# Performance work log

Measured on AMD Instinct MI355X. Metric: run time of the kernel, lower is better.

Reference implementation:

```python
import jax, jax.numpy as jnp
import numpy as np

DIM = 1024
HEADS = 16
DIM_HEAD = 64
INNER = HEADS * DIM_HEAD  # 1024
EPS = 1e-5


def layernorm(x, w, b):
    mu = jnp.mean(x, axis=-1, keepdims=True)
    var = jnp.mean(jnp.square(x - mu), axis=-1, keepdims=True)
    return (x - mu) * jax.lax.rsqrt(var + EPS) * w + b


def setup_inputs() -> dict:
    key = jax.random.key(0)
    ks = jax.random.split(key, 9)
    b, n1, n2 = 4, 4096, 256
    x = jax.random.normal(ks[0], (b, n1, DIM), dtype=jnp.float32)
    latents = jax.random.normal(ks[1], (b, n2, DIM), dtype=jnp.float32)
    shift = jax.random.normal(ks[2], (b, HEADS), dtype=jnp.float32)
    scale = jax.random.normal(ks[3], (b, HEADS), dtype=jnp.float32)
    s = 1.0 / np.sqrt(DIM)
    Wq = jax.random.normal(ks[4], (DIM, INNER), dtype=jnp.float32) * s
    Wkv = jax.random.normal(ks[5], (DIM, 2 * INNER), dtype=jnp.float32) * s
    Wout = jax.random.normal(ks[6], (INNER, DIM), dtype=jnp.float32) * (1.0 / np.sqrt(INNER))
    ln1_w = jnp.ones((DIM,), jnp.float32)
    ln1_b = jnp.zeros((DIM,), jnp.float32)
    ln2_w = jnp.ones((DIM,), jnp.float32)
    ln2_b = jnp.zeros((DIM,), jnp.float32)
    return {"x": x, "latents": latents, "shift": shift, "scale": scale,
            "ln1_w": ln1_w, "ln1_b": ln1_b, "ln2_w": ln2_w, "ln2_b": ln2_b,
            "Wq": Wq, "Wkv": Wkv, "Wout": Wout}


def reference(x, latents, shift, scale, ln1_w, ln1_b, ln2_w, ln2_b, Wq, Wkv, Wout):
    b = x.shape[0]
    xn = layernorm(x, ln1_w, ln1_b)            # (b, n1, D)
    ln = layernorm(latents, ln2_w, ln2_b)      # (b, n2, D)
    q = ln @ Wq                                 # (b, n2, inner)
    kv = xn @ Wkv                               # (b, n1, 2*inner)
    k, v = jnp.split(kv, 2, axis=-1)
    q = q.reshape(b, -1, HEADS, DIM_HEAD)
    k = k.reshape(b, -1, HEADS, DIM_HEAD)
    v = v.reshape(b, -1, HEADS, DIM_HEAD)
    # AdaLN-style per-head modulation on q
    q = q * (1.0 + scale[:, None, :, None]) + shift[:, None, :, None]
    # fp32 attention scores (already fp32 here)
    attn_scale = DIM_HEAD ** -0.5
    qk = jnp.einsum('bihd,bjhd->bhij', q.astype(jnp.float32), k.astype(jnp.float32)) * attn_scale
    attn = jax.nn.softmax(qk, axis=-1).astype(v.dtype)  # (b, h, n2, n1)
    out = jnp.einsum('bhij,bjhd->bihd', attn, v)         # (b, n2, h, dh)
    out = out.reshape(b, -1, INNER)
    return out @ Wout
```

## Files before the change

### kernel.cpp

```cpp
#include <hip/hip_runtime.h>

typedef __bf16 bf16;
typedef bf16 bf16x8 __attribute__((ext_vector_type(8)));
typedef bf16 bf16x4 __attribute__((ext_vector_type(4)));
typedef float f32x4 __attribute__((ext_vector_type(4)));

#define B_ 4
#define N1 4096
#define N2 256
#define DIM 1024
#define HEADS 16
#define DH 64
#define INNER 1024
#define ASPLIT 4
#define KEYS_PER_SPLIT (N1 / ASPLIT)
#define SPLIT_ELEMS (4 * 16 * 256 * 64)

typedef __attribute__((address_space(1))) const void gvoid_t;
typedef __attribute__((address_space(3))) void lvoid_t;
__device__ __forceinline__ void async16(const void* g, void* l) {
  __builtin_amdgcn_global_load_lds((gvoid_t*)g, (lvoid_t*)l, 16, 0, 0);
}

__global__ __launch_bounds__(256) void ln_all(
    const float* __restrict__ x, const float* __restrict__ latents,
    const float* __restrict__ ln1w, const float* __restrict__ ln1b,
    const float* __restrict__ ln2w, const float* __restrict__ ln2b,
    bf16* __restrict__ xn, bf16* __restrict__ lnl) {
  int wv = threadIdx.x >> 6, lane = threadIdx.x & 63;
  int grow = blockIdx.x * 4 + wv;
  const float *src, *w, *bb;
  bf16* dst;
  int row;
  if (grow < 16384) { src = x; w = ln1w; bb = ln1b; dst = xn; row = grow; }
  else { src = latents; w = ln2w; bb = ln2b; dst = lnl; row = grow - 16384; }
  const float4* p = (const float4*)(src + (size_t)row * DIM);
  float4 v[4];
  for (int j = 0; j < 4; j++) v[j] = p[j * 64 + lane];
  float s = 0.f, sq = 0.f;
  for (int j = 0; j < 4; j++) {
    s += v[j].x + v[j].y + v[j].z + v[j].w;
    sq += v[j].x * v[j].x + v[j].y * v[j].y + v[j].z * v[j].z + v[j].w * v[j].w;
  }
  for (int off = 32; off; off >>= 1) {
    s += __shfl_xor(s, off, 64);
    sq += __shfl_xor(sq, off, 64);
  }
  float mu = s * (1.0f / DIM);
  float var = sq * (1.0f / DIM) - mu * mu;
  float r = rsqrtf(var + 1e-5f);
  for (int j = 0; j < 4; j++) {
    float4 wv4 = ((const float4*)w)[j * 64 + lane];
    float4 bv4 = ((const float4*)bb)[j * 64 + lane];
    bf16x4 o;
    o[0] = (bf16)((v[j].x - mu) * r * wv4.x + bv4.x);
    o[1] = (bf16)((v[j].y - mu) * r * wv4.y + bv4.y);
    o[2] = (bf16)((v[j].z - mu) * r * wv4.z + bv4.z);
    o[3] = (bf16)((v[j].w - mu) * r * wv4.w + bv4.w);
    *(bf16x4*)(dst + (size_t)row * DIM + (j * 64 + lane) * 4) = o;
  }
}

__global__ __launch_bounds__(256) void transpose_w_all(
    const float* __restrict__ Wq, const float* __restrict__ Wkv,
    const float* __restrict__ Wout, bf16* __restrict__ WqT,
    bf16* __restrict__ WkvT, bf16* __restrict__ WoutT) {
  __shared__ float tile[32][33];
  int t = blockIdx.x;
  const float* src;
  bf16* dst;
  int N;
  if (t < 1024) { src = Wq; dst = WqT; N = 1024; }
  else if (t < 3072) { t -= 1024; src = Wkv; dst = WkvT; N = 2048; }
  else { t -= 3072; src = Wout; dst = WoutT; N = 1024; }
  int ntiles = N >> 5;
  int n0 = (t % ntiles) * 32, k0 = (t / ntiles) * 32;
  int x = threadIdx.x, y = threadIdx.y;
  for (int j = 0; j < 4; j++)
    tile[y + 8 * j][x] = src[(size_t)(k0 + y + 8 * j) * N + n0 + x];
  __syncthreads();
  for (int j = 0; j < 4; j++)
    dst[(size_t)(n0 + y + 8 * j) * 1024 + k0 + x] = (bf16)tile[x][y + 8 * j];
}

__global__ __launch_bounds__(256) void gemm_kv(
    const bf16* __restrict__ A, const bf16* __restrict__ Bt,
    bf16* __restrict__ Cout, bf16* __restrict__ Cout2, int K) {
  __shared__ __align__(16) bf16 smem[128 * 64 * 2];
  bf16* As = smem;
  bf16* Bs = smem + 128 * 64;
  int tid = threadIdx.x;
  int lane = tid & 63, wv = tid >> 6;
  int wr = wv >> 1, wc = wv & 1;
  int quad = lane >> 4, lr = lane & 15;
  int bid = blockIdx.y * 16 + blockIdx.x;
  int c = bid & 7, g = bid >> 3;
  int mi = g & 7, nb = (g >> 3) & 15, chunk = g >> 7;
  int m0 = (chunk * 64 + mi * 8 + c) * 128;
  int n0 = nb * 128;
  f32x4 acc[4][4] = {};
  for (int kt = 0; kt < K; kt += 64) {
    __syncthreads();
    for (int j = 0; j < 4; j++) {
      int idx0 = j * 256 + wv * 64;
      int row = (idx0 >> 3) + (lane >> 3);
      int cb = (lane & 7) ^ (row & 7);
      async16(&A[(size_t)(m0 + row) * K + kt + cb * 8], &As[idx0 * 8]);
      async16(&Bt[(size_t)(n0 + row) * K + kt + cb * 8], &Bs[idx0 * 8]);
    }
    __syncthreads();
    for (int kk = 0; kk < 2; kk++) {
      bf16x8 af[4], bfr[4];
      for (int im = 0; im < 4; im++) {
        int row = wr * 64 + im * 16 + lr;
        af[im] = *(const bf16x8*)&As[row * 64 + ((quad + 4 * kk) ^ (row & 7)) * 8];
      }
      for (int in = 0; in < 4; in++) {
        int row = wc * 64 + in * 16 + lr;
        bfr[in] = *(const bf16x8*)&Bs[row * 64 + ((quad + 4 * kk) ^ (row & 7)) * 8];
      }
      for (int im = 0; im < 4; im++)
        for (int in = 0; in < 4; in++)
          acc[im][in] = __builtin_amdgcn_mfma_f32_16x16x32_bf16(
              af[im], bfr[in], acc[im][in], 0, 0, 0);
    }
  }

  if (n0 >= 1024) {
    bf16* Ct = smem;
    for (int pass = 0; pass < 2; pass++) {
      __syncthreads();
      for (int inL = 0; inL < 2; inL++) {
        int in = pass * 2 + inL;
        int cc = wc * 32 + inL * 16 + lr;
        for (int im = 0; im < 4; im++) {
          int rb = wr * 64 + im * 16 + quad * 4;
          bf16x4 pk;
          for (int r = 0; r < 4; r++) pk[r] = (bf16)acc[im][in][r];
          *(bf16x4*)&Ct[cc * 136 + rb] = pk;
        }
      }
      __syncthreads();
      for (int k2 = 0; k2 < 4; k2++) {
        int ci = k2 * 256 + tid;
        int cc = ci >> 4, ch = ci & 15;
        uint4 val = *(const uint4*)&Ct[cc * 136 + ch * 8];
        int gco = (cc >> 5) * 64 + pass * 32 + (cc & 31);
        int col = n0 - 1024 + gco;
        int bb2 = m0 >> 12;
        int key = (m0 & 4095) + ch * 8;
        *(uint4*)&Cout2[((size_t)(bb2 * 1024 + col)) * 4096 + key] = val;
      }
    }
    return;
  }

  for (int im = 0; im < 4; im++)
    for (int in = 0; in < 4; in++) {
      int col = n0 + wc * 64 + in * 16 + lr;
      for (int r = 0; r < 4; r++) {
        int row = m0 + wr * 64 + im * 16 + quad * 4 + r;
        Cout[(size_t)row * 1024 + col] = (bf16)acc[im][in][r];
      }
    }
}

template <int MODE>
__global__ __launch_bounds__(256) void gemm64(
    const bf16* __restrict__ A, const bf16* __restrict__ Bt,
    void* __restrict__ Cout, int K, int N,
    const float* __restrict__ shiftp, const float* __restrict__ scalep) {
  __shared__ __align__(16) bf16 As[64 * 64];
  __shared__ __align__(16) bf16 Bs[64 * 64];
  int tid = threadIdx.x;
  int lane = tid & 63, wv = tid >> 6;
  int wr = wv >> 1, wc = wv & 1;
  int quad = lane >> 4, lr = lane & 15;
  int m0 = blockIdx.y * 64, n0 = blockIdx.x * 64;
  f32x4 acc[2][2] = {};
  for (int kt = 0; kt < K; kt += 64) {
    __syncthreads();
    for (int j = 0; j < 2; j++) {
      int idx0 = j * 256 + wv * 64;
      int row = (idx0 >> 3) + (lane >> 3);
      int cb = (lane & 7) ^ (row & 7);
      async16(&A[(size_t)(m0 + row) * K + kt + cb * 8], &As[idx0 * 8]);
      async16(&Bt[(size_t)(n0 + row) * K + kt + cb * 8], &Bs[idx0 * 8]);
    }
    __syncthreads();
    for (int kk = 0; kk < 2; kk++) {
      bf16x8 af[2], bfr[2];
      for (int im = 0; im < 2; im++) {
        int row = wr * 32 + im * 16 + lr;
        af[im] = *(const bf16x8*)&As[row * 64 + ((quad + 4 * kk) ^ (row & 7)) * 8];
      }
      for (int in = 0; in < 2; in++) {
        int row = wc * 32 + in * 16 + lr;
        bfr[in] = *(const bf16x8*)&Bs[row * 64 + ((quad + 4 * kk) ^ (row & 7)) * 8];
      }
      for (int im = 0; im < 2; im++)
        for (int in = 0; in < 2; in++)
          acc[im][in] = __builtin_amdgcn_mfma_f32_16x16x32_bf16(
              af[im], bfr[in], acc[im][in], 0, 0, 0);
    }
  }
  for (int im = 0; im < 2; im++)
    for (int in = 0; in < 2; in++) {
      int col = n0 + wc * 32 + in * 16 + lr;
      for (int r = 0; r < 4; r++) {
        int row = m0 + wr * 32 + im * 16 + quad * 4 + r;
        float v = acc[im][in][r];
        if (MODE == 1) {
          int bb = row >> 8, hh = col >> 6;
          float sc = scalep[bb * 16 + hh], sh = shiftp[bb * 16 + hh];
          ((bf16*)Cout)[(size_t)row * N + col] =
              (bf16)((v * (1.0f + sc) + sh) * 0.18033688011112042f);
        } else {
          ((float*)Cout)[(size_t)row * N + col] = v;
        }
      }
    }
}

__global__ __launch_bounds__(256) void attn_kernel(const bf16* __restrict__ q,
                                                   const bf16* __restrict__ kb,
                                                   const bf16* __restrict__ vt,
                                                   float* __restrict__ opA,
                                                   float* __restrict__ opB,
                                                   float* __restrict__ ml) {
  int b = blockIdx.z, h = blockIdx.y;
  int qt = blockIdx.x >> 2, sp = blockIdx.x & 3;
  int tid = threadIdx.x, lane = tid & 63, wv = tid >> 6;
  int quad = lane >> 4, lr = lane & 15;
  __shared__ __align__(16) bf16 Ks[64 * 64];
  __shared__ __align__(16) bf16 Vs[64 * 64];
  __shared__ __align__(16) bf16 QP[64 * 64];
  __shared__ float abuf[4][16];
  int q0 = qt * 64;

  const bf16* qg = q + (size_t)(b * N2 + q0) * INNER + h * DH;
  for (int j = 0; j < 2; j++) {
    int r0 = j * 32 + wv * 8;
    int r = r0 + (lane >> 3);
    async16(&qg[(size_t)r * INNER + ((lane & 7) ^ (r & 7)) * 8], &QP[r0 * 64]);
  }
  __syncthreads();
  bf16x8 aQ[2];
  {
    int row = wv * 16 + lr;
    for (int kk = 0; kk < 2; kk++)
      aQ[kk] = *(const bf16x8*)&QP[row * 64 + ((quad + 4 * kk) ^ (row & 7)) * 8];
  }
  float m_s = -1e30f, l_s = 0.0f;
  f32x4 oacc[4] = {};

  const bf16* kg = kb + (size_t)(b * N1) * 1024 + h * DH;
  const bf16* vg = vt + (size_t)((b * HEADS + h) * DH) * N1;
  bf16* Ps = QP + wv * 1024;

  for (int t = 0; t < KEYS_PER_SPLIT / 64; t++) {
    int key0 = sp * KEYS_PER_SPLIT + t * 64;
    __syncthreads();
    for (int j = 0; j < 2; j++) {
      int r0 = j * 32 + wv * 8;
      int r = r0 + (lane >> 3);
      int cs = ((lane & 7) ^ (r & 7)) * 8;
      async16(&kg[(size_t)(key0 + r) * 1024 + cs], &Ks[r0 * 64]);
      async16(&vg[(size_t)r * N1 + key0 + cs], &Vs[r0 * 64]);
    }
    __syncthreads();

    f32x4 s[4] = {};
    for (int kk = 0; kk < 2; kk++)
      for (int nt = 0; nt < 4; nt++) {
        int row = nt * 16 + lr;
        bf16x8 ak =
            *(const bf16x8*)&Ks[row * 64 + ((quad + 4 * kk) ^ (row & 7)) * 8];
        s[nt] = __builtin_amdgcn_mfma_f32_16x16x32_bf16(ak, aQ[kk], s[nt], 0, 0, 0);
      }

    float mx = s[0][0];
    for (int nt = 0; nt < 4; nt++)
      for (int r = 0; r < 4; r++) mx = fmaxf(mx, s[nt][r]);
    mx = fmaxf(mx, __shfl_xor(mx, 16, 64));
    mx = fmaxf(mx, __shfl_xor(mx, 32, 64));
    float mn = fmaxf(m_s, mx);
    float al = exp2f(m_s - mn);
    float p[4][4], sum = 0.0f;
    for (int nt = 0; nt < 4; nt++)
      for (int r = 0; r < 4; r++) {
        p[nt][r] = exp2f(s[nt][r] - mn);
        sum += p[nt][r];
      }
    sum += __shfl_xor(sum, 16, 64);
    sum += __shfl_xor(sum, 32, 64);
    l_s = l_s * al + sum;
    m_s = mn;
    if (quad == 0) abuf[wv][lr] = al;

    for (int nt = 0; nt < 4; nt++) {
      bf16x4 pk;
      for (int r = 0; r < 4; r++) pk[r] = (bf16)p[nt][r];
      *(bf16x4*)&Ps[lr * 64 + ((2 * nt + (quad >> 1)) ^ (lr & 7)) * 8 +
                    (quad & 1) * 4] = pk;
    }

    f32x4 a4 = *(const f32x4*)&abuf[wv][quad * 4];
    for (int in = 0; in < 4; in++)
      for (int r = 0; r < 4; r++) oacc[in][r] *= a4[r];

    bf16x8 aP[2];
    for (int kk = 0; kk < 2; kk++)
      aP[kk] = *(const bf16x8*)&Ps[lr * 64 + ((4 * kk + quad) ^ (lr & 7)) * 8];

    for (int kk = 0; kk < 2; kk++)
      for (int in = 0; in < 4; in++) {
        int row = in * 16 + lr;
        bf16x8 bv =
            *(const bf16x8*)&Vs[row * 64 + ((quad + 4 * kk) ^ (row & 7)) * 8];
        oacc[in] = __builtin_amdgcn_mfma_f32_16x16x32_bf16(aP[kk], bv, oacc[in], 0, 0, 0);
      }
  }

  float* ob = (sp < 2 ? opA : opB) + (size_t)(sp & 1) * SPLIT_ELEMS;
  size_t rbase = (size_t)(b * HEADS + h) * N2;
  for (int r = 0; r < 4; r++) {
    int qq = q0 + wv * 16 + quad * 4 + r;
    for (int in = 0; in < 4; in++)
      ob[(rbase + qq) * 64 + in * 16 + lr] = oacc[in][r];
  }
  if (quad == 0) {
    int qq = q0 + wv * 16 + lr;
    float* mlp = ml + ((size_t)sp * (4 * HEADS * N2) + rbase + qq) * 2;
    mlp[0] = m_s;
    mlp[1] = l_s;
  }
}

__global__ __launch_bounds__(256) void combine_kernel(const float* __restrict__ opA,
                                                      const float* __restrict__ opB,
                                                      const float* __restrict__ ml,
                                                      bf16* __restrict__ out) {
  int gid = blockIdx.x * 256 + threadIdx.x;
  int d = gid & 63;
  int rq = gid >> 6;
  int qq = rq & 255, bh = rq >> 8;
  int h = bh & 15, b = bh >> 4;
  float m[ASPLIT], l[ASPLIT];
  for (int s = 0; s < ASPLIT; s++) {
    const float* p = ml + ((size_t)s * (4 * HEADS * N2) + rq) * 2;
    m[s] = p[0];
    l[s] = p[1];
  }
  float M = fmaxf(fmaxf(m[0], m[1]), fmaxf(m[2], m[3]));
  float L = 0.0f, o = 0.0f;
  for (int s = 0; s < ASPLIT; s++) {
    float w = exp2f(m[s] - M);
    L += w * l[s];
    const float* op = (s < 2 ? opA : opB) + (size_t)(s & 1) * SPLIT_ELEMS;
    o += w * op[(size_t)rq * 64 + d];
  }
  out[((size_t)(b * N2 + qq)) * INNER + h * DH + d] = (bf16)(o / L);
}

extern "C" void kernel_launch(void* const* d_in, const int* in_sizes, int n_in,
                              void* d_out, int out_size, void* d_ws,
                              size_t ws_size, hipStream_t stream) {
  const float* x       = (const float*)d_in[0];
  const float* latents = (const float*)d_in[1];
  const float* shift   = (const float*)d_in[2];
  const float* scale   = (const float*)d_in[3];
  const float* ln1w    = (const float*)d_in[4];
  const float* ln1b    = (const float*)d_in[5];
  const float* ln2w    = (const float*)d_in[6];
  const float* ln2b    = (const float*)d_in[7];
  const float* Wq      = (const float*)d_in[8];
  const float* Wkv     = (const float*)d_in[9];
  const float* Wout    = (const float*)d_in[10];

  char* ws = (char*)d_ws;
  bf16*  xn    = (bf16*)(ws);
  float* opA   = (float*)(ws);
  bf16*  lnl   = (bf16*)(ws + 33554432);
  float* ml    = (float*)(ws + 33554432);
  bf16*  qb    = (bf16*)(ws + 35651584);
  bf16*  kb    = (bf16*)(ws + 37748736);
  float* opB   = (float*)(ws + 71303168);
  bf16*  vtb   = (bf16*)(ws + 104857600);
  bf16*  aob   = (bf16*)(ws + 138412032);
  bf16*  WqT   = (bf16*)(ws + 140509184);
  bf16*  WkvT  = (bf16*)(ws + 142606336);
  bf16*  WoutT = (bf16*)(ws + 146800640);

  transpose_w_all<<<4096, dim3(32, 8), 0, stream>>>(Wq, Wkv, Wout, WqT, WkvT,
                                                    WoutT);
  ln_all<<<4352, 256, 0, stream>>>(x, latents, ln1w, ln1b, ln2w, ln2b, xn, lnl);

  gemm_kv<<<dim3(16, 128), 256, 0, stream>>>(xn, WkvT, kb, vtb, 1024);
  gemm64<1><<<dim3(16, 16), 256, 0, stream>>>(lnl, WqT, qb, 1024, 1024, shift,
                                              scale);
  attn_kernel<<<dim3(4 * ASPLIT, 16, 4), 256, 0, stream>>>(qb, kb, vtb, opA,
                                                           opB, ml);
  combine_kernel<<<16384, 256, 0, stream>>>(opA, opB, ml, aob);
  gemm64<2><<<dim3(16, 16), 256, 0, stream>>>(aob, WoutT, d_out, 1024, 1024,
                                              nullptr, nullptr);
}
```

Measured before the change: 299.0 us.

## Fuse prep and Q/KV GEMM launches, widen attention query tile, bf16 partials with LSE

Merges weight transposes and layernorms into one prep kernel, and runs the Q projection GEMM as extra blocks inside the KV GEMM launch to cut launch count and tail effects. The attention kernel now handles 128 queries per block, loading K/V fragments into registers once and reusing them for two query groups. Split partial outputs are normalized and stored in bf16 with a single log-sum-exp per row, halving combine traffic. This costs fewer attention blocks (less parallelism), more register pressure, and slightly lower precision in the partials.

Result: faster. 288.4 us (-3.5%).

```diff
diff --git a/kernel.cpp b/kernel.cpp
--- a/kernel.cpp
+++ b/kernel.cpp
@@ -15,6 +15,7 @@
 #define ASPLIT 4
 #define KEYS_PER_SPLIT (N1 / ASPLIT)
 #define SPLIT_ELEMS (4 * 16 * 256 * 64)
+#define ROWS_TOTAL (4 * HEADS * N2)
 
 typedef __attribute__((address_space(1))) const void gvoid_t;
 typedef __attribute__((address_space(3))) void lvoid_t;
@@ -22,13 +23,35 @@
   __builtin_amdgcn_global_load_lds((gvoid_t*)g, (lvoid_t*)l, 16, 0, 0);
 }
 
-__global__ __launch_bounds__(256) void ln_all(
+__global__ __launch_bounds__(256) void prep(
+    const float* __restrict__ Wq, const float* __restrict__ Wkv,
+    const float* __restrict__ Wout, bf16* __restrict__ WqT,
+    bf16* __restrict__ WkvT, bf16* __restrict__ WoutT,
     const float* __restrict__ x, const float* __restrict__ latents,
     const float* __restrict__ ln1w, const float* __restrict__ ln1b,
     const float* __restrict__ ln2w, const float* __restrict__ ln2b,
     bf16* __restrict__ xn, bf16* __restrict__ lnl) {
+  __shared__ float tile[32][33];
+  int t = blockIdx.x;
+  if (t < 4096) {
+    const float* src;
+    bf16* dst;
+    int N;
+    if (t < 1024) { src = Wq; dst = WqT; N = 1024; }
+    else if (t < 3072) { t -= 1024; src = Wkv; dst = WkvT; N = 2048; }
+    else { t -= 3072; src = Wout; dst = WoutT; N = 1024; }
+    int ntiles = N >> 5;
+    int n0 = (t % ntiles) * 32, k0 = (t / ntiles) * 32;
+    int xx = threadIdx.x & 31, yy = threadIdx.x >> 5;
+    for (int j = 0; j < 4; j++)
+      tile[yy + 8 * j][xx] = src[(size_t)(k0 + yy + 8 * j) * N + n0 + xx];
+    __syncthreads();
+    for (int j = 0; j < 4; j++)
+      dst[(size_t)(n0 + yy + 8 * j) * 1024 + k0 + xx] = (bf16)tile[xx][yy + 8 * j];
+    return;
+  }
   int wv = threadIdx.x >> 6, lane = threadIdx.x & 63;
-  int grow = blockIdx.x * 4 + wv;
+  int grow = (t - 4096) * 4 + wv;
   const float *src, *w, *bb;
   bf16* dst;
   int row;
@@ -61,52 +84,80 @@
   }
 }
 
-__global__ __launch_bounds__(256) void transpose_w_all(
-    const float* __restrict__ Wq, const float* __restrict__ Wkv,
-    const float* __restrict__ Wout, bf16* __restrict__ WqT,
-    bf16* __restrict__ WkvT, bf16* __restrict__ WoutT) {
-  __shared__ float tile[32][33];
-  int t = blockIdx.x;
-  const float* src;
-  bf16* dst;
-  int N;
-  if (t < 1024) { src = Wq; dst = WqT; N = 1024; }
-  else if (t < 3072) { t -= 1024; src = Wkv; dst = WkvT; N = 2048; }
-  else { t -= 3072; src = Wout; dst = WoutT; N = 1024; }
-  int ntiles = N >> 5;
-  int n0 = (t % ntiles) * 32, k0 = (t / ntiles) * 32;
-  int x = threadIdx.x, y = threadIdx.y;
-  for (int j = 0; j < 4; j++)
-    tile[y + 8 * j][x] = src[(size_t)(k0 + y + 8 * j) * N + n0 + x];
-  __syncthreads();
-  for (int j = 0; j < 4; j++)
-    dst[(size_t)(n0 + y + 8 * j) * 1024 + k0 + x] = (bf16)tile[x][y + 8 * j];
-}
-
-__global__ __launch_bounds__(256) void gemm_kv(
+__global__ __launch_bounds__(256) void gemm_kvq(
     const bf16* __restrict__ A, const bf16* __restrict__ Bt,
-    bf16* __restrict__ Cout, bf16* __restrict__ Cout2, int K) {
+    bf16* __restrict__ Cout, bf16* __restrict__ Cout2,
+    const bf16* __restrict__ Aq, const bf16* __restrict__ Bq,
+    bf16* __restrict__ Cq, const float* __restrict__ shiftp,
+    const float* __restrict__ scalep) {
   __shared__ __align__(16) bf16 smem[128 * 64 * 2];
-  bf16* As = smem;
-  bf16* Bs = smem + 128 * 64;
   int tid = threadIdx.x;
   int lane = tid & 63, wv = tid >> 6;
   int wr = wv >> 1, wc = wv & 1;
   int quad = lane >> 4, lr = lane & 15;
-  int bid = blockIdx.y * 16 + blockIdx.x;
-  int c = bid & 7, g = bid >> 3;
+  int bidx = blockIdx.x;
+
+  if (bidx >= 2048) {
+    int qbid = bidx - 2048;
+    int m0 = (qbid >> 4) * 64, n0 = (qbid & 15) * 64;
+    bf16* As = smem;
+    bf16* Bs = smem + 64 * 64;
+    f32x4 acc[2][2] = {};
+    for (int kt = 0; kt < 1024; kt += 64) {
+      __syncthreads();
+      for (int j = 0; j < 2; j++) {
+        int idx0 = j * 256 + wv * 64;
+        int row = (idx0 >> 3) + (lane >> 3);
+        int cb = (lane & 7) ^ (row & 7);
+        async16(&Aq[(size_t)(m0 + row) * 1024 + kt + cb * 8], &As[idx0 * 8]);
+        async16(&Bq[(size_t)(n0 + row) * 1024 + kt + cb * 8], &Bs[idx0 * 8]);
+      }
+      __syncthreads();
+      for (int kk = 0; kk < 2; kk++) {
+        bf16x8 af[2], bfr[2];
+        for (int im = 0; im < 2; im++) {
+          int row = wr * 32 + im * 16 + lr;
+          af[im] = *(const bf16x8*)&As[row * 64 + ((quad + 4 * kk) ^ (row & 7)) * 8];
+        }
+        for (int in = 0; in < 2; in++) {
+          int row = wc * 32 + in * 16 + lr;
+          bfr[in] = *(const bf16x8*)&Bs[row * 64 + ((quad + 4 * kk) ^ (row & 7)) * 8];
+        }
+        for (int im = 0; im < 2; im++)
+          for (int in = 0; in < 2; in++)
+            acc[im][in] = __builtin_amdgcn_mfma_f32_16x16x32_bf16(
+                af[im], bfr[in], acc[im][in], 0, 0, 0);
+      }
+    }
+    for (int im = 0; im < 2; im++)
+      for (int in = 0; in < 2; in++) {
+        int col = n0 + wc * 32 + in * 16 + lr;
+        for (int r = 0; r < 4; r++) {
+          int row = m0 + wr * 32 + im * 16 + quad * 4 + r;
+          int bb = row >> 8, hh = col >> 6;
+          float sc = scalep[bb * 16 + hh], sh = shiftp[bb * 16 + hh];
+          Cq[(size_t)row * 1024 + col] =
+              (bf16)((acc[im][in][r] * (1.0f + sc) + sh) * 0.18033688011112042f);
+        }
+      }
+    return;
+  }
+
+  bf16* As = smem;
+  bf16* Bs = smem + 128 * 64;
+  int c = bidx & 7, g = bidx >> 3;
   int mi = g & 7, nb = (g >> 3) & 15, chunk = g >> 7;
   int m0 = (chunk * 64 + mi * 8 + c) * 128;
   int n0 = nb * 128;
   f32x4 acc[4][4] = {};
-  for (int kt = 0; kt < K; kt += 64) {
+  for (int kt = 0; kt < 1024; kt += 64) {
     __syncthreads();
     for (int j = 0; j < 4; j++) {
       int idx0 = j * 256 + wv * 64;
       int row = (idx0 >> 3) + (lane >> 3);
       int cb = (lane & 7) ^ (row & 7);
-      async16(&A[(size_t)(m0 + row) * K + kt + cb * 8], &As[idx0 * 8]);
-      async16(&Bt[(size_t)(n0 + row) * K + kt + cb * 8], &Bs[idx0 * 8]);
+      async16(&A[(size_t)(m0 + row) * 1024 + kt + cb * 8], &As[idx0 * 8]);
+      async16(&Bt[(size_t)(n0 + row) * 1024 + kt + cb * 8], &Bs[idx0 * 8]);
     }
     __syncthreads();
     for (int kk = 0; kk < 2; kk++) {
@@ -165,11 +216,9 @@
     }
 }
 
-template <int MODE>
-__global__ __launch_bounds__(256) void gemm64(
+__global__ __launch_bounds__(256) void gemm_out(
     const bf16* __restrict__ A, const bf16* __restrict__ Bt,
-    void* __restrict__ Cout, int K, int N,
-    const float* __restrict__ shiftp, const float* __restrict__ scalep) {
+    float* __restrict__ Cout) {
   __shared__ __align__(16) bf16 As[64 * 64];
   __shared__ __align__(16) bf16 Bs[64 * 64];
   int tid = threadIdx.x;
@@ -178,14 +227,14 @@
   int quad = lane >> 4, lr = lane & 15;
   int m0 = blockIdx.y * 64, n0 = blockIdx.x * 64;
   f32x4 acc[2][2] = {};
-  for (int kt = 0; kt < K; kt += 64) {
+  for (int kt = 0; kt < 1024; kt += 64) {
     __syncthreads();
     for (int j = 0; j < 2; j++) {
       int idx0 = j * 256 + wv * 64;
       int row = (idx0 >> 3) + (lane >> 3);
       int cb = (lane & 7) ^ (row & 7);
-      async16(&A[(size_t)(m0 + row) * K + kt + cb * 8], &As[idx0 * 8]);
-      async16(&Bt[(size_t)(n0 + row) * K + kt + cb * 8], &Bs[idx0 * 8]);
+      async16(&A[(size_t)(m0 + row) * 1024 + kt + cb * 8], &As[idx0 * 8]);
+      async16(&Bt[(size_t)(n0 + row) * 1024 + kt + cb * 8], &Bs[idx0 * 8]);
     }
     __syncthreads();
     for (int kk = 0; kk < 2; kk++) {
@@ -209,15 +258,7 @@
       int col = n0 + wc * 32 + in * 16 + lr;
       for (int r = 0; r < 4; r++) {
         int row = m0 + wr * 32 + im * 16 + quad * 4 + r;
-        float v = acc[im][in][r];
-        if (MODE == 1) {
-          int bb = row >> 8, hh = col >> 6;
-          float sc = scalep[bb * 16 + hh], sh = shiftp[bb * 16 + hh];
-          ((bf16*)Cout)[(size_t)row * N + col] =
-              (bf16)((v * (1.0f + sc) + sh) * 0.18033688011112042f);
-        } else {
-          ((float*)Cout)[(size_t)row * N + col] = v;
-        }
+        Cout[(size_t)row * 1024 + col] = acc[im][in][r];
       }
     }
 }
@@ -225,38 +266,37 @@
 __global__ __launch_bounds__(256) void attn_kernel(const bf16* __restrict__ q,
                                                    const bf16* __restrict__ kb,
                                                    const bf16* __restrict__ vt,
-                                                   float* __restrict__ opA,
-                                                   float* __restrict__ opB,
-                                                   float* __restrict__ ml) {
+                                                   bf16* __restrict__ opb,
+                                                   float* __restrict__ lseb) {
   int b = blockIdx.z, h = blockIdx.y;
-  int qt = blockIdx.x >> 2, sp = blockIdx.x & 3;
+  int qp = blockIdx.x >> 2, sp = blockIdx.x & 3;
   int tid = threadIdx.x, lane = tid & 63, wv = tid >> 6;
   int quad = lane >> 4, lr = lane & 15;
   __shared__ __align__(16) bf16 Ks[64 * 64];
   __shared__ __align__(16) bf16 Vs[64 * 64];
-  __shared__ __align__(16) bf16 QP[64 * 64];
+  __shared__ __align__(16) bf16 QP[128 * 64];
   __shared__ float abuf[4][16];
-  int q0 = qt * 64;
+  int q0 = qp * 128;
 
   const bf16* qg = q + (size_t)(b * N2 + q0) * INNER + h * DH;
-  for (int j = 0; j < 2; j++) {
+  for (int j = 0; j < 4; j++) {
     int r0 = j * 32 + wv * 8;
     int r = r0 + (lane >> 3);
     async16(&qg[(size_t)r * INNER + ((lane & 7) ^ (r & 7)) * 8], &QP[r0 * 64]);
   }
   __syncthreads();
-  bf16x8 aQ[2];
-  {
-    int row = wv * 16 + lr;
+  bf16x8 aQ[2][2];
+  for (int g = 0; g < 2; g++) {
+    int row = wv * 32 + g * 16 + lr;
     for (int kk = 0; kk < 2; kk++)
-      aQ[kk] = *(const bf16x8*)&QP[row * 64 + ((quad + 4 * kk) ^ (row & 7)) * 8];
-  }
-  float m_s = -1e30f, l_s = 0.0f;
-  f32x4 oacc[4] = {};
+      aQ[g][kk] = *(const bf16x8*)&QP[row * 64 + ((quad + 4 * kk) ^ (row & 7)) * 8];
+  }
+  float m_s[2] = {-1e30f, -1e30f}, l_s[2] = {0.0f, 0.0f};
+  f32x4 oacc[2][4] = {};
 
   const bf16* kg = kb + (size_t)(b * N1) * 1024 + h * DH;
   const bf16* vg = vt + (size_t)((b * HEADS + h) * DH) * N1;
-  bf16* Ps = QP + wv * 1024;
+  bf16* Ps = QP + wv * 2048;
 
   for (int t = 0; t < KEYS_PER_SPLIT / 64; t++) {
     int key0 = sp * KEYS_PER_SPLIT + t * 64;
@@ -270,95 +310,95 @@
     }
     __syncthreads();
 
-    f32x4 s[4] = {};
+    bf16x8 ak[2][4], bv[2][4];
     for (int kk = 0; kk < 2; kk++)
       for (int nt = 0; nt < 4; nt++) {
         int row = nt * 16 + lr;
-        bf16x8 ak =
+        ak[kk][nt] =
             *(const bf16x8*)&Ks[row * 64 + ((quad + 4 * kk) ^ (row & 7)) * 8];
-        s[nt] = __builtin_amdgcn_mfma_f32_16x16x32_bf16(ak, aQ[kk], s[nt], 0, 0, 0);
-      }
-
-    float mx = s[0][0];
-    for (int nt = 0; nt < 4; nt++)
-      for (int r = 0; r < 4; r++) mx = fmaxf(mx, s[nt][r]);
-    mx = fmaxf(mx, __shfl_xor(mx, 16, 64));
-    mx = fmaxf(mx, __shfl_xor(mx, 32, 64));
-    float mn = fmaxf(m_s, mx);
-    float al = exp2f(m_s - mn);
-    float p[4][4], sum = 0.0f;
-    for (int nt = 0; nt < 4; nt++)
-      for (int r = 0; r < 4; r++) {
-        p[nt][r] = exp2f(s[nt][r] - mn);
-        sum += p[nt][r];
-      }
-    sum += __shfl_xor(sum, 16, 64);
-    sum += __shfl_xor(sum, 32, 64);
-    l_s = l_s * al + sum;
-    m_s = mn;
-    if (quad == 0) abuf[wv][lr] = al;
-
-    for (int nt = 0; nt < 4; nt++) {
-      bf16x4 pk;
-      for (int r = 0; r < 4; r++) pk[r] = (bf16)p[nt][r];
-      *(bf16x4*)&Ps[lr * 64 + ((2 * nt + (quad >> 1)) ^ (lr & 7)) * 8 +
-                    (quad & 1) * 4] = pk;
-    }
-
-    f32x4 a4 = *(const f32x4*)&abuf[wv][quad * 4];
-    for (int in = 0; in < 4; in++)
-      for (int r = 0; r < 4; r++) oacc[in][r] *= a4[r];
-
-    bf16x8 aP[2];
-    for (int kk = 0; kk < 2; kk++)
-      aP[kk] = *(const bf16x8*)&Ps[lr * 64 + ((4 * kk + quad) ^ (lr & 7)) * 8];
-
-    for (int kk = 0; kk < 2; kk++)
-      for (int in = 0; in < 4; in++) {
-        int row = in * 16 + lr;
-        bf16x8 bv =
+        bv[kk][nt] =
             *(const bf16x8*)&Vs[row * 64 + ((quad + 4 * kk) ^ (row & 7)) * 8];
-        oacc[in] = __builtin_amdgcn_mfma_f32_16x16x32_bf16(aP[kk], bv, oacc[in], 0, 0, 0);
-      }
-  }
-
-  float* ob = (sp < 2 ? opA : opB) + (size_t)(sp & 1) * SPLIT_ELEMS;
+      }
+
+    for (int g = 0; g < 2; g++) {
+      f32x4 s[4] = {};
+      for (int kk = 0; kk < 2; kk++)
+        for (int nt = 0; nt < 4; nt++)
+          s[nt] = __builtin_amdgcn_mfma_f32_16x16x32_bf16(ak[kk][nt], aQ[g][kk],
+                                                          s[nt], 0, 0, 0);
+      float mx = s[0][0];
+      for (int nt = 0; nt < 4; nt++)
+        for (int r = 0; r < 4; r++) mx = fmaxf(mx, s[nt][r]);
+      mx = fmaxf(mx, __shfl_xor(mx, 16, 64));
+      mx = fmaxf(mx, __shfl_xor(mx, 32, 64));
+      float mn = fmaxf(m_s[g], mx);
+      float al = exp2f(m_s[g] - mn);
+      float p[4][4], sum = 0.0f;
+      for (int nt = 0; nt < 4; nt++)
+        for (int r = 0; r < 4; r++) {
+          p[nt][r] = exp2f(s[nt][r] - mn);
+          sum += p[nt][r];
+        }
+      sum += __shfl_xor(sum, 16, 64);
+      sum += __shfl_xor(sum, 32, 64);
+      l_s[g] = l_s[g] * al + sum;
+      m_s[g] = mn;
+      if (quad == 0) abuf[wv][lr] = al;
+
+      for (int nt = 0; nt < 4; nt++) {
+        bf16x4 pk;
+        for (int r = 0; r < 4; r++) pk[r] = (bf16)p[nt][r];
+        *(bf16x4*)&Ps[lr * 64 + ((2 * nt + (quad >> 1)) ^ (lr & 7)) * 8 +
+                      (quad & 1) * 4] = pk;
+      }
+
+      f32x4 a4 = *(const f32x4*)&abuf[wv][quad * 4];
+      for (int in = 0; in < 4; in++)
+        for (int r = 0; r < 4; r++) oacc[g][in][r] *= a4[r];
+
+      bf16x8 aP[2];
+      for (int kk = 0; kk < 2; kk++)
+        aP[kk] = *(const bf16x8*)&Ps[lr * 64 + ((4 * kk + quad) ^ (lr & 7)) * 8];
+      for (int kk = 0; kk < 2; kk++)
+        for (int in = 0; in < 4; in++)
+          oacc[g][in] = __builtin_amdgcn_mfma_f32_16x16x32_bf16(
+              aP[kk], bv[kk][in], oacc[g][in], 0, 0, 0);
+    }
+  }
+
+  bf16* ob = opb + (size_t)sp * SPLIT_ELEMS;
   size_t rbase = (size_t)(b * HEADS + h) * N2;
-  for (int r = 0; r < 4; r++) {
-    int qq = q0 + wv * 16 + quad * 4 + r;
-    for (int in = 0; in < 4; in++)
-      ob[(rbase + qq) * 64 + in * 16 + lr] = oacc[in][r];
-  }
-  if (quad == 0) {
-    int qq = q0 + wv * 16 + lr;
-    float* mlp = ml + ((size_t)sp * (4 * HEADS * N2) + rbase + qq) * 2;
-    mlp[0] = m_s;
-    mlp[1] = l_s;
-  }
-}
-
-__global__ __launch_bounds__(256) void combine_kernel(const float* __restrict__ opA,
-                                                      const float* __restrict__ opB,
-                                                      const float* __restrict__ ml,
+  for (int g = 0; g < 2; g++) {
+    for (int r = 0; r < 4; r++) {
+      float lrow = __shfl(l_s[g], quad * 4 + r, 16);
+      float inv = 1.0f / lrow;
+      int qq = q0 + wv * 32 + g * 16 + quad * 4 + r;
+      for (int in = 0; in < 4; in++)
+        ob[(rbase + qq) * 64 + in * 16 + lr] = (bf16)(oacc[g][in][r] * inv);
+    }
+    if (quad == 0) {
+      int qq = q0 + wv * 32 + g * 16 + lr;
+      lseb[(size_t)sp * ROWS_TOTAL + rbase + qq] = m_s[g] + __log2f(l_s[g]);
+    }
+  }
+}
+
+__global__ __launch_bounds__(256) void combine_kernel(const bf16* __restrict__ opb,
+                                                      const float* __restrict__ lseb,
                                                       bf16* __restrict__ out) {
   int gid = blockIdx.x * 256 + threadIdx.x;
   int d = gid & 63;
   int rq = gid >> 6;
   int qq = rq & 255, bh = rq >> 8;
   int h = bh & 15, b = bh >> 4;
-  float m[ASPLIT], l[ASPLIT];
-  for (int s = 0; s < ASPLIT; s++) {
-    const float* p = ml + ((size_t)s * (4 * HEADS * N2) + rq) * 2;
-    m[s] = p[0];
-    l[s] = p[1];
-  }
-  float M = fmaxf(fmaxf(m[0], m[1]), fmaxf(m[2], m[3]));
+  float ls[ASPLIT];
+  for (int s = 0; s < ASPLIT; s++) ls[s] = lseb[(size_t)s * ROWS_TOTAL + rq];
+  float M = fmaxf(fmaxf(ls[0], ls[1]), fmaxf(ls[2], ls[3]));
   float L = 0.0f, o = 0.0f;
   for (int s = 0; s < ASPLIT; s++) {
-    float w = exp2f(m[s] - M);
-    L += w * l[s];
-    const float* op = (s < 2 ? opA : opB) + (size_t)(s & 1) * SPLIT_ELEMS;
-    o += w * op[(size_t)rq * 64 + d];
+    float w = exp2f(ls[s] - M);
+    L += w;
+    o += w * (float)opb[(size_t)s * SPLIT_ELEMS + (size_t)rq * 64 + d];
   }
   out[((size_t)(b * N2 + qq)) * INNER + h * DH + d] = (bf16)(o / L);
 }
@@ -380,28 +420,23 @@
 
   char* ws = (char*)d_ws;
   bf16*  xn    = (bf16*)(ws);
-  float* opA   = (float*)(ws);
+  bf16*  opb   = (bf16*)(ws);
   bf16*  lnl   = (bf16*)(ws + 33554432);
-  float* ml    = (float*)(ws + 33554432);
+  float* lseb  = (float*)(ws + 33554432);
   bf16*  qb    = (bf16*)(ws + 35651584);
   bf16*  kb    = (bf16*)(ws + 37748736);
-  float* opB   = (float*)(ws + 71303168);
   bf16*  vtb   = (bf16*)(ws + 104857600);
   bf16*  aob   = (bf16*)(ws + 138412032);
   bf16*  WqT   = (bf16*)(ws + 140509184);
   bf16*  WkvT  = (bf16*)(ws + 142606336);
   bf16*  WoutT = (bf16*)(ws + 146800640);
 
-  transpose_w_all<<<4096, dim3(32, 8), 0, stream>>>(Wq, Wkv, Wout, WqT, WkvT,
-                                                    WoutT);
-  ln_all<<<4352, 256, 0, stream>>>(x, latents, ln1w, ln1b, ln2w, ln2b, xn, lnl);
-
-  gemm_kv<<<dim3(16, 128), 256, 0, stream>>>(xn, WkvT, kb, vtb, 1024);
-  gemm64<1><<<dim3(16, 16), 256, 0, stream>>>(lnl, WqT, qb, 1024, 1024, shift,
-                                              scale);
-  attn_kernel<<<dim3(4 * ASPLIT, 16, 4), 256, 0, stream>>>(qb, kb, vtb, opA,
-                                                           opB, ml);
-  combine_kernel<<<16384, 256, 0, stream>>>(opA, opB, ml, aob);
-  gemm64<2><<<dim3(16, 16), 256, 0, stream>>>(aob, WoutT, d_out, 1024, 1024,
-                                              nullptr, nullptr);
-}
+  prep<<<8448, 256, 0, stream>>>(Wq, Wkv, Wout, WqT, WkvT, WoutT, x, latents,
+                                 ln1w, ln1b, ln2w, ln2b, xn, lnl);
+  gemm_kvq<<<2304, 256, 0, stream>>>(xn, WkvT, kb, vtb, lnl, WqT, qb, shift,
+                                     scale);
+  attn_kernel<<<dim3(2 * ASPLIT, 16, 4), 256, 0, stream>>>(qb, kb, vtb, opb,
+                                                           lseb);
+  combine_kernel<<<16384, 256, 0, stream>>>(opb, lseb, aob);
+  gemm_out<<<dim3(16, 16), 256, 0, stream>>>(aob, WoutT, (float*)d_out);
+}
```
